# Performance work log

Measured on AMD Instinct MI355X. Metric: run time of the kernel, lower is better.

Reference implementation:

```python
import jax, jax.numpy as jnp
import numpy as np
from jax import lax

NUM_KP = 17
MAX_PEOPLE = 30
HEAT_THRESH = 0.1
STRIDE = 4  # heatmap -> image coordinate scale

def setup_inputs() -> dict:
    key = jax.random.key(0)
    heatmaps = jax.random.uniform(key, (32, NUM_KP, 256, 256), dtype=jnp.float32)
    return {"heatmaps": heatmaps}

def reference(heatmaps):
    # heatmaps: [B, C, H, W]
    B, C, H, W = heatmaps.shape
    neg_inf = jnp.float32(-jnp.inf)
    # 3x3 max-pool NMS (stride 1, pad 1) batched over all B*C channels at once.
    hmax = lax.reduce_window(
        heatmaps, neg_inf, lax.max,
        window_dimensions=(1, 1, 3, 3),
        window_strides=(1, 1, 1, 1),
        padding=((0, 0), (0, 0), (1, 1), (1, 1)),
    )
    nms = heatmaps * (hmax == heatmaps).astype(heatmaps.dtype)
    # Threshold + descending sort + take top max_people, done as a batched top_k.
    flat = nms.reshape(B, C, H * W)
    masked = jnp.where(flat > HEAT_THRESH, flat, neg_inf)
    scores, idx = lax.top_k(masked, MAX_PEOPLE)          # [B, C, max_people]
    y = idx // W
    x = idx % W
    coords = jnp.stack([x, y], axis=-1).astype(jnp.int32) * STRIDE  # [B,C,max_people,2] as (x,y)*4
    valid = scores > HEAT_THRESH                          # padding mask (original output is ragged)
    return coords, scores, valid
```

## Files before the change

kernel.cpp:

```cpp
#include <hip/hip_runtime.h>
#include <stdint.h>

#define NUM_KP 17
#define BATCH  32
#define HDIM   256
#define WDIM   256
#define NCH    (BATCH * NUM_KP)
#define MAXP   30
#define CAP    8192

#define NBINS  4096
#define QB     125953

#define THREADS 512

__device__ __forceinline__ unsigned long long shfl_down_u64(unsigned long long v, int off) {
    unsigned lo = (unsigned)v, hi = (unsigned)(v >> 32);
    lo = __shfl_down(lo, off);
    hi = __shfl_down(hi, off);
    return ((unsigned long long)hi << 32) | lo;
}
__device__ __forceinline__ unsigned long long shfl_u64(unsigned long long v, int lane) {
    unsigned lo = (unsigned)v, hi = (unsigned)(v >> 32);
    lo = __shfl(lo, lane);
    hi = __shfl(hi, lane);
    return ((unsigned long long)hi << 32) | lo;
}
__device__ __forceinline__ unsigned quant12(float v) {
    int b = (int)(__float_as_uint(v) >> 13) - QB;
    b = b < 1 ? 1 : (b > NBINS - 1 ? NBINS - 1 : b);
    return (unsigned)b;
}

__global__ __launch_bounds__(THREADS, 4)
void pose_fused_kernel(const float* __restrict__ heat, float* __restrict__ out, int out_size) {
    __shared__ unsigned s_buf[CAP];
    __shared__ int s_hist[NBINS];
    __shared__ int s_gsum[256];
    __shared__ unsigned long long s_ref[256];
    __shared__ int s_cnt, s_nref, s_tau;

    const int tid  = threadIdx.x;
    const int chan = blockIdx.x;
    const int wave = tid >> 6;
    const int lane = tid & 63;
    const float NEGINF = -__builtin_inff();
    const float* __restrict__ cp = heat + (size_t)chan * (HDIM * WDIM);

    for (int i = tid; i < NBINS; i += THREADS) s_hist[i] = 0;
    if (tid == 0) { s_cnt = 0; s_nref = 0; }
    __syncthreads();

    const int r0 = wave << 5;
    const float* colp = cp + (lane << 2);
    const float4 NEG4 = make_float4(NEGINF, NEGINF, NEGINF, NEGINF);
    const unsigned long long ltmask = (1ull << lane) - 1ull;

    auto LD = [&](int r) -> float4 {
        return (r >= 0 && r < HDIM) ? *(const float4*)(colp + (r << 8)) : NEG4;
    };

    auto process = [&](const float4& up, const float4& md, const float4& dn, int r) {
        float vm0 = fmaxf(up.x, fmaxf(md.x, dn.x));
        float vm1 = fmaxf(up.y, fmaxf(md.y, dn.y));
        float vm2 = fmaxf(up.z, fmaxf(md.z, dn.z));
        float vm3 = fmaxf(up.w, fmaxf(md.w, dn.w));
        float left  = __shfl_up(vm3, 1);   if (lane == 0)  left  = NEGINF;
        float right = __shfl_down(vm0, 1); if (lane == 63) right = NEGINF;
        float h0 = fmaxf(left, fmaxf(vm0, vm1));
        float h1 = fmaxf(vm0, fmaxf(vm1, vm2));
        float h2 = fmaxf(vm1, fmaxf(vm2, vm3));
        float h3 = fmaxf(vm2, fmaxf(vm3, right));

        bool p0 = md.x > 0.1f && md.x == h0;
        bool p1 = md.y > 0.1f && md.y == h1;
        bool p2 = md.z > 0.1f && md.z == h2;
        bool p3 = md.w > 0.1f && md.w == h3;
        unsigned long long b0 = __ballot(p0), b1 = __ballot(p1);
        unsigned long long b2 = __ballot(p2), b3 = __ballot(p3);
        int c0 = __popcll(b0), c1 = __popcll(b1), c2 = __popcll(b2), c3 = __popcll(b3);
        int tot = c0 + c1 + c2 + c3;
        int wb = 0;
        if (lane == 0 && tot > 0) wb = atomicAdd(&s_cnt, tot);
        wb = __shfl(wb, 0);

        const int base = (r << 8) | (lane << 2);
        if (p0) { int pos = wb + __popcll(b0 & ltmask);
                  if (pos < CAP) s_buf[pos] = (quant12(md.x) << 16) | (unsigned)(base + 0); }
        if (p1) { int pos = wb + c0 + __popcll(b1 & ltmask);
                  if (pos < CAP) s_buf[pos] = (quant12(md.y) << 16) | (unsigned)(base + 1); }
        if (p2) { int pos = wb + c0 + c1 + __popcll(b2 & ltmask);
                  if (pos < CAP) s_buf[pos] = (quant12(md.z) << 16) | (unsigned)(base + 2); }
        if (p3) { int pos = wb + c0 + c1 + c2 + __popcll(b3 & ltmask);
                  if (pos < CAP) s_buf[pos] = (quant12(md.w) << 16) | (unsigned)(base + 3); }
    };

    float4 rm   = LD(r0 - 1);
    float4 cur0 = LD(r0 + 0), cur1 = LD(r0 + 1), cur2 = LD(r0 + 2), cur3 = LD(r0 + 3);

    #pragma unroll
    for (int g = 0; g < 8; ++g) {
        const int rb = r0 + (g << 2);
        float4 n0, n1, n2, n3;
        if (g < 7) {
            n0 = LD(rb + 4); n1 = LD(rb + 5); n2 = LD(rb + 6); n3 = LD(rb + 7);
        } else {
            n0 = LD(rb + 4); n1 = NEG4; n2 = NEG4; n3 = NEG4;
        }
        process(rm,   cur0, cur1, rb + 0);
        process(cur0, cur1, cur2, rb + 1);
        process(cur1, cur2, cur3, rb + 2);
        process(cur2, cur3, n0,   rb + 3);
        rm = cur3; cur0 = n0; cur1 = n1; cur2 = n2; cur3 = n3;
    }
    __syncthreads();

    const int n = s_cnt < CAP ? s_cnt : CAP;
    for (int i = tid; i < n; i += THREADS) {
        atomicAdd(&s_hist[s_buf[i] >> 16], 1);
    }
    __syncthreads();

    if (tid < 256) {
        int s = 0;
        #pragma unroll
        for (int j = 0; j < 16; ++j) s += s_hist[tid * 16 + j];
        s_gsum[tid] = s;
    }
    __syncthreads();
    if (tid == 0) {
        int cum = 0, tau = 0;
        for (int g = 255; g >= 0; --g) {
            int gs = s_gsum[g];
            if (cum + gs >= MAXP) {
                for (int b = g * 16 + 15; b >= g * 16; --b) {
                    cum += s_hist[b];
                    if (cum >= MAXP) { tau = b; break; }
                }
                break;
            }
            cum += gs;
        }
        s_tau = tau;
    }
    __syncthreads();

    const unsigned tau = (unsigned)s_tau;
    for (int i = tid; i < n; i += THREADS) {
        unsigned p = s_buf[i];
        if ((p >> 16) >= tau) {
            int pos = atomicAdd(&s_nref, 1);
            if (pos < 256) {
                unsigned idx = p & 0xFFFFu;
                float sc = cp[idx];
                s_ref[pos] = ((unsigned long long)__float_as_uint(sc) << 32) | (unsigned)(~idx);
            }
        }
    }
    __syncthreads();
    const int nref = s_nref < 256 ? s_nref : 256;

    if (tid < 64) {
        unsigned long long k0 = (tid       < nref) ? s_ref[tid]       : 0ull;
        unsigned long long k1 = (tid + 64  < nref) ? s_ref[tid + 64]  : 0ull;
        unsigned long long k2 = (tid + 128 < nref) ? s_ref[tid + 128] : 0ull;
        unsigned long long k3 = (tid + 192 < nref) ? s_ref[tid + 192] : 0ull;
        for (int r = 0; r < MAXP; ++r) {
            unsigned long long best = k0; int bs = 0;
            if (k1 > best) { best = k1; bs = 1; }
            if (k2 > best) { best = k2; bs = 2; }
            if (k3 > best) { best = k3; bs = 3; }
            unsigned long long key = best;
            int slot = (bs << 6) | tid;
            #pragma unroll
            for (int off = 32; off > 0; off >>= 1) {
                unsigned long long ok = shfl_down_u64(key, off);
                int os = __shfl_down(slot, off);
                if (ok > key) { key = ok; slot = os; }
            }
            key  = shfl_u64(key, 0);
            slot = __shfl(slot, 0);
            if ((slot & 63) == tid) {
                int which = slot >> 6;
                if      (which == 0) k0 = 0ull;
                else if (which == 1) k1 = 0ull;
                else if (which == 2) k2 = 0ull;
                else                 k3 = 0ull;
            }
            if (tid == 0) {
                float sc, vld; unsigned idx;
                if (key != 0ull) {
                    sc  = __uint_as_float((unsigned)(key >> 32));
                    idx = (~(unsigned)key) & 0xFFFFu;
                    vld = 1.0f;
                } else { sc = NEGINF; idx = 0u; vld = 0.0f; }
                int x = (int)(idx & 255), y = (int)(idx >> 8);
                long long cb = ((long long)chan * MAXP + r) * 2;
                if (cb + 1 < out_size) {
                    out[cb]     = (float)(x * 4);
                    out[cb + 1] = (float)(y * 4);
                }
                long long so = (long long)NCH * MAXP * 2 + (long long)chan * MAXP + r;
                if (so < out_size) out[so] = sc;
                long long vo = (long long)NCH * MAXP * 3 + (long long)chan * MAXP + r;
                if (vo < out_size) out[vo] = vld;
            }
        }
    }
}

extern "C" void kernel_launch(void* const* d_in, const int* in_sizes, int n_in,
                              void* d_out, int out_size, void* d_ws, size_t ws_size,
                              hipStream_t stream) {
    const float* heat = (const float*)d_in[0];
    float* out = (float*)d_out;
    hipLaunchKernelGGL(pose_fused_kernel, dim3(NCH), dim3(THREADS), 0, stream, heat, out, out_size);
}
```

Baseline: 238.1 us.

## Use per-wave candidate segments, packed 16-bit histogram, and wave-parallel threshold scan

```diff
diff --git a/kernel.cpp b/kernel.cpp
--- a/kernel.cpp
+++ b/kernel.cpp
@@ -7,12 +7,12 @@
 #define WDIM   256
 #define NCH    (BATCH * NUM_KP)
 #define MAXP   30
-#define CAP    8192
+#define THREADS 512
+#define NWAVES  8
+#define SEGCAP  1280
 
 #define NBINS  4096
 #define QB     125953
-
-#define THREADS 512
 
 __device__ __forceinline__ unsigned long long shfl_down_u64(unsigned long long v, int off) {
     unsigned lo = (unsigned)v, hi = (unsigned)(v >> 32);
@@ -32,13 +32,14 @@
     return (unsigned)b;
 }
 
-__global__ __launch_bounds__(THREADS, 4)
+__global__ __launch_bounds__(THREADS, 6)
 void pose_fused_kernel(const float* __restrict__ heat, float* __restrict__ out, int out_size) {
-    __shared__ unsigned s_buf[CAP];
-    __shared__ int s_hist[NBINS];
+    __shared__ unsigned s_buf[NWAVES * SEGCAP];
+    __shared__ unsigned s_hist[NBINS / 2];
     __shared__ int s_gsum[256];
     __shared__ unsigned long long s_ref[256];
-    __shared__ int s_cnt, s_nref, s_tau;
+    __shared__ int s_wcnt[NWAVES];
+    __shared__ int s_nref, s_tau;
 
     const int tid  = threadIdx.x;
     const int chan = blockIdx.x;
@@ -47,19 +48,27 @@
     const float NEGINF = -__builtin_inff();
     const float* __restrict__ cp = heat + (size_t)chan * (HDIM * WDIM);
 
-    for (int i = tid; i < NBINS; i += THREADS) s_hist[i] = 0;
-    if (tid == 0) { s_cnt = 0; s_nref = 0; }
+    for (int i = tid; i < NBINS / 2; i += THREADS) s_hist[i] = 0;
+    if (tid == 0) s_nref = 0;
     __syncthreads();
 
     const int r0 = wave << 5;
     const float* colp = cp + (lane << 2);
     const float4 NEG4 = make_float4(NEGINF, NEGINF, NEGINF, NEGINF);
     const unsigned long long ltmask = (1ull << lane) - 1ull;
+    unsigned* __restrict__ seg = s_buf + wave * SEGCAP;
+    int wavecnt = 0;
 
     auto LD = [&](int r) -> float4 {
         return (r >= 0 && r < HDIM) ? *(const float4*)(colp + (r << 8)) : NEG4;
     };
-
+    auto push = [&](float v, int pidx, int pos) {
+        if (pos < SEGCAP) {
+            unsigned q = quant12(v);
+            seg[pos] = (q << 16) | (unsigned)pidx;
+            atomicAdd(&s_hist[q >> 1], 1u << ((q & 1) << 4));
+        }
+    };
     auto process = [&](const float4& up, const float4& md, const float4& dn, int r) {
         float vm0 = fmaxf(up.x, fmaxf(md.x, dn.x));
         float vm1 = fmaxf(up.y, fmaxf(md.y, dn.y));
@@ -78,82 +87,92 @@
         bool p3 = md.w > 0.1f && md.w == h3;
         unsigned long long b0 = __ballot(p0), b1 = __ballot(p1);
         unsigned long long b2 = __ballot(p2), b3 = __ballot(p3);
-        int c0 = __popcll(b0), c1 = __popcll(b1), c2 = __popcll(b2), c3 = __popcll(b3);
-        int tot = c0 + c1 + c2 + c3;
-        int wb = 0;
-        if (lane == 0 && tot > 0) wb = atomicAdd(&s_cnt, tot);
-        wb = __shfl(wb, 0);
+        int c0 = __popcll(b0), c1 = __popcll(b1), c2 = __popcll(b2);
+        int before = wavecnt;
+        wavecnt += c0 + c1 + c2 + __popcll(b3);
 
         const int base = (r << 8) | (lane << 2);
-        if (p0) { int pos = wb + __popcll(b0 & ltmask);
-                  if (pos < CAP) s_buf[pos] = (quant12(md.x) << 16) | (unsigned)(base + 0); }
-        if (p1) { int pos = wb + c0 + __popcll(b1 & ltmask);
-                  if (pos < CAP) s_buf[pos] = (quant12(md.y) << 16) | (unsigned)(base + 1); }
-        if (p2) { int pos = wb + c0 + c1 + __popcll(b2 & ltmask);
-                  if (pos < CAP) s_buf[pos] = (quant12(md.z) << 16) | (unsigned)(base + 2); }
-        if (p3) { int pos = wb + c0 + c1 + c2 + __popcll(b3 & ltmask);
-                  if (pos < CAP) s_buf[pos] = (quant12(md.w) << 16) | (unsigned)(base + 3); }
+        if (p0) push(md.x, base + 0, before + __popcll(b0 & ltmask));
+        if (p1) push(md.y, base + 1, before + c0 + __popcll(b1 & ltmask));
+        if (p2) push(md.z, base + 2, before + c0 + c1 + __popcll(b2 & ltmask));
+        if (p3) push(md.w, base + 3, before + c0 + c1 + c2 + __popcll(b3 & ltmask));
     };
 
     float4 rm   = LD(r0 - 1);
     float4 cur0 = LD(r0 + 0), cur1 = LD(r0 + 1), cur2 = LD(r0 + 2), cur3 = LD(r0 + 3);
-
     #pragma unroll
     for (int g = 0; g < 8; ++g) {
         const int rb = r0 + (g << 2);
         float4 n0, n1, n2, n3;
-        if (g < 7) {
-            n0 = LD(rb + 4); n1 = LD(rb + 5); n2 = LD(rb + 6); n3 = LD(rb + 7);
-        } else {
-            n0 = LD(rb + 4); n1 = NEG4; n2 = NEG4; n3 = NEG4;
-        }
+        if (g < 7) { n0 = LD(rb + 4); n1 = LD(rb + 5); n2 = LD(rb + 6); n3 = LD(rb + 7); }
+        else       { n0 = LD(rb + 4); n1 = NEG4; n2 = NEG4; n3 = NEG4; }
         process(rm,   cur0, cur1, rb + 0);
         process(cur0, cur1, cur2, rb + 1);
         process(cur1, cur2, cur3, rb + 2);
         process(cur2, cur3, n0,   rb + 3);
         rm = cur3; cur0 = n0; cur1 = n1; cur2 = n2; cur3 = n3;
     }
-    __syncthreads();
-
-    const int n = s_cnt < CAP ? s_cnt : CAP;
-    for (int i = tid; i < n; i += THREADS) {
-        atomicAdd(&s_hist[s_buf[i] >> 16], 1);
-    }
+    if (lane == 0) s_wcnt[wave] = wavecnt < SEGCAP ? wavecnt : SEGCAP;
     __syncthreads();
 
     if (tid < 256) {
         int s = 0;
         #pragma unroll
-        for (int j = 0; j < 16; ++j) s += s_hist[tid * 16 + j];
+        for (int j = 0; j < 8; ++j) {
+            unsigned w = s_hist[tid * 8 + j];
+            s += (int)(w & 0xFFFFu) + (int)(w >> 16);
+        }
         s_gsum[tid] = s;
     }
     __syncthreads();
-    if (tid == 0) {
-        int cum = 0, tau = 0;
-        for (int g = 255; g >= 0; --g) {
-            int gs = s_gsum[g];
-            if (cum + gs >= MAXP) {
-                for (int b = g * 16 + 15; b >= g * 16; --b) {
-                    cum += s_hist[b];
+    if (wave == 0) {
+        int u0 = s_gsum[(lane << 2) + 0], u1 = s_gsum[(lane << 2) + 1];
+        int u2 = s_gsum[(lane << 2) + 2], u3 = s_gsum[(lane << 2) + 3];
+        int t = u0 + u1 + u2 + u3;
+        int R = t;
+        #pragma unroll
+        for (int off = 1; off < 64; off <<= 1) {
+            int v = __shfl_down(R, off);
+            if (lane + off < 64) R += v;
+        }
+        int E = R - t;
+        int sg3 = u3 + E, sg2 = u2 + sg3, sg1 = u1 + sg2, sg0 = u0 + sg1;
+        unsigned long long mask = __ballot(sg0 >= MAXP);
+        if (mask == 0ull) {
+            if (lane == 0) s_tau = 0;
+        } else {
+            int hi = 63 - __builtin_clzll(mask);
+            if (lane == hi) {
+                int k, above;
+                if      (sg3 >= MAXP) { k = 3; above = E;   }
+                else if (sg2 >= MAXP) { k = 2; above = sg3; }
+                else if (sg1 >= MAXP) { k = 1; above = sg2; }
+                else                  { k = 0; above = sg1; }
+                int g = (lane << 2) + k;
+                int cum = above, tau = 0;
+                for (int b = (g << 4) + 15; b >= (g << 4); --b) {
+                    cum += (int)((s_hist[b >> 1] >> ((b & 1) << 4)) & 0xFFFFu);
                     if (cum >= MAXP) { tau = b; break; }
                 }
-                break;
-            }
-            cum += gs;
-        }
-        s_tau = tau;
+                s_tau = tau;
+            }
+        }
     }
     __syncthreads();
 
     const unsigned tau = (unsigned)s_tau;
-    for (int i = tid; i < n; i += THREADS) {
-        unsigned p = s_buf[i];
-        if ((p >> 16) >= tau) {
-            int pos = atomicAdd(&s_nref, 1);
-            if (pos < 256) {
-                unsigned idx = p & 0xFFFFu;
-                float sc = cp[idx];
-                s_ref[pos] = ((unsigned long long)__float_as_uint(sc) << 32) | (unsigned)(~idx);
+    for (int s = 0; s < NWAVES; ++s) {
+        const int c = s_wcnt[s];
+        const unsigned* sb = s_buf + s * SEGCAP;
+        for (int i = tid; i < c; i += THREADS) {
+            unsigned p = sb[i];
+            if ((p >> 16) >= tau) {
+                int pos = atomicAdd(&s_nref, 1);
+                if (pos < 256) {
+                    unsigned idx = p & 0xFFFFu;
+                    float sc = cp[idx];
+                    s_ref[pos] = ((unsigned long long)__float_as_uint(sc) << 32) | (unsigned)(~idx);
+                }
             }
         }
     }
```

After: 238.4 us. Within noise of the previous version (+0.1%).
